# Kernel optimization log

Measured on AMD Instinct MI355X. Metric: run time of the kernel, lower is better.

The kernel has to match this reference:

```python
import jax, jax.numpy as jnp
import numpy as np

U1, U2, FEAT = 24, 48, 16
LN_EPS = 1e-3  # tf.keras LayerNormalization default


def _ln(x, gamma, beta):
    mu = jnp.mean(x, axis=-1, keepdims=True)
    var = jnp.mean(jnp.square(x - mu), axis=-1, keepdims=True)
    return (x - mu) * jax.lax.rsqrt(var + LN_EPS) * gamma + beta


def setup_inputs() -> dict:
    key = jax.random.key(0)
    ks = jax.random.split(key, 8)
    B, T = 8192, 256
    sequence = jax.random.normal(ks[0], (B, T, FEAT), dtype=jnp.float32)
    s = 0.1
    return {
        "sequence": sequence,
        "W1": jax.random.normal(ks[1], (FEAT, U1), dtype=jnp.float32) * s,
        "b1": jnp.zeros((U1,), jnp.float32),
        "Wr1": jax.random.normal(ks[2], (U1, U1), dtype=jnp.float32) * s,
        "br1": jnp.zeros((U1,), jnp.float32),
        "g1": jnp.ones((U1,), jnp.float32),
        "be1": jnp.zeros((U1,), jnp.float32),
        "W2": jax.random.normal(ks[3], (U1, U2), dtype=jnp.float32) * s,
        "b2": jnp.zeros((U2,), jnp.float32),
        "Wr2": jax.random.normal(ks[4], (U2, U2), dtype=jnp.float32) * s,
        "br2": jnp.zeros((U2,), jnp.float32),
        "g2": jnp.ones((U2,), jnp.float32),
        "be2": jnp.zeros((U2,), jnp.float32),
        "Wout": jax.random.normal(ks[5], (U2, 1), dtype=jnp.float32) * s,
        "bout": jnp.zeros((1,), jnp.float32),
    }


def reference(sequence, W1, b1, Wr1, br1, g1, be1, W2, b2, Wr2, br2, g2, be2, Wout, bout):
    B = sequence.shape[0]
    xs = jnp.swapaxes(sequence, 0, 1)  # [T, B, F]

    def step(carry, inp):
        s1, s2 = carry
        x = inp @ W1 + b1 + s1
        ns1 = jnp.tanh(x @ Wr1 + br1)
        h = _ln(ns1, g1, be1)
        y = h @ W2 + b2 + s2
        ns2 = jnp.tanh(y @ Wr2 + br2)
        return (ns1, ns2), None

    init = (jnp.zeros((B, U1), sequence.dtype), jnp.zeros((B, U2), sequence.dtype))
    (s1, s2), _ = jax.lax.scan(step, init, xs)
    last_out = _ln(s2, g2, be2)  # output of final timestep (return_sequences=False)
    return jax.nn.sigmoid(last_out @ Wout + bout)  # [B, 1]
```

## Files before the change

kernel.cpp:

```cpp
#include <hip/hip_runtime.h>

#define T_STEPS 256
#define FEAT 16
#define U1 24
#define U2 48
#define ROWB 144
#define SLOTS 8

typedef short bf16x8 __attribute__((ext_vector_type(8)));
typedef float f32x4 __attribute__((ext_vector_type(4)));

__device__ __forceinline__ unsigned short f2bf(float f) {
    unsigned u = __float_as_uint(f);
    u += 0x7fffu + ((u >> 16) & 1u);
    return (unsigned short)(u >> 16);
}

#if defined(__has_builtin)
#if __has_builtin(__builtin_amdgcn_cvt_pk_bf16_f32)
#define HAVE_PKBF16 1
#endif
#endif

__device__ __forceinline__ unsigned pk2(float a, float b) {
#ifdef HAVE_PKBF16
    typedef __bf16 bf2 __attribute__((ext_vector_type(2)));
    union { bf2 v; unsigned u; } cv;
    cv.v = __builtin_amdgcn_cvt_pk_bf16_f32(a, b);
    return cv.u;
#else
    return (unsigned)f2bf(a) | ((unsigned)f2bf(b) << 16);
#endif
}
__device__ __forceinline__ float bfr(float x) {
    return __uint_as_float(((unsigned)f2bf(x)) << 16);
}
__device__ __forceinline__ float fast_tanh(float z) {
    return 1.0f - 2.0f / (1.0f + __expf(2.0f * z));
}

union FragU { bf16x8 v; unsigned u[4]; };

#define MFMA(A, B, C) __builtin_amdgcn_mfma_f32_16x16x32_bf16((A), (B), (C), 0, 0, 0)

__device__ __forceinline__ void bar_sync() {
    asm volatile("" ::: "memory");
    __builtin_amdgcn_s_waitcnt(0xC07F);
    __builtin_amdgcn_s_barrier();
    asm volatile("" ::: "memory");
}

__global__ __launch_bounds__(128) void rnn_kernel(
    const float* __restrict__ seq,
    const float* __restrict__ W1, const float* __restrict__ b1,
    const float* __restrict__ Wr1, const float* __restrict__ br1,
    const float* __restrict__ g1, const float* __restrict__ be1,
    const float* __restrict__ W2, const float* __restrict__ b2,
    const float* __restrict__ Wr2, const float* __restrict__ br2,
    const float* __restrict__ g2, const float* __restrict__ be2,
    const float* __restrict__ Wout, const float* __restrict__ bout,
    float* __restrict__ out)
{
    __shared__ __align__(16) unsigned char tr0[16 * ROWB];
    __shared__ __align__(16) unsigned char tr1[16 * ROWB];
    __shared__ __align__(16) unsigned char ring[SLOTS * 16 * ROWB];

    const int tid = threadIdx.x;
    const int w = tid >> 6;
    const int lane = tid & 63;
    const int j15 = lane & 15;
    const int g = lane >> 4;
    const f32x4 z4 = {0.f, 0.f, 0.f, 0.f};

    if (w == 0) {
        bf16x8 A1[2], A2[2];
#pragma unroll
        for (int t = 0; t < 2; ++t) {
            const int m = 16 * t + j15;
            FragU f1, f2;
#pragma unroll
            for (int j = 0; j < 8; ++j) {
                const int k = 8 * g + j;
                float v1 = 0.f, v2 = 0.f;
                if (m < U1) {
                    if (k < FEAT) v1 = W1[k * U1 + m];
                    else if (k == FEAT) v1 = b1[m];
                    if (k < U1) v2 = Wr1[k * U1 + m];
                    else if (k == U1) v2 = br1[m];
                } else if (m == U1 && k == FEAT) {
                    v1 = 1.f;
                }
                f1.v[j] = (short)f2bf(v1);
                f2.v[j] = (short)f2bf(v2);
            }
            A1[t] = f1.v; A2[t] = f2.v;
        }
        const unsigned cdw0 = (g == 2) ? 0x00003F80u : 0u;
        unsigned char* const xrow = tr0 + j15 * ROWB;

        const float* sp = seq + (size_t)(blockIdx.x * 16 + j15) * (T_STEPS * FEAT) + 8 * g;
        const bool ld = (lane < 32);

        f32x4 s1[2] = {z4, z4};

        auto pstep = [&](int t, const float4 ca, const float4 cb) {
            FragU inf;
            const unsigned p0 = pk2(ca.x, ca.y), p1 = pk2(ca.z, ca.w);
            const unsigned p2 = pk2(cb.x, cb.y), p3 = pk2(cb.z, cb.w);
            const bool lo = (g < 2);
            inf.u[0] = lo ? p0 : cdw0;
            inf.u[1] = lo ? p1 : 0u;
            inf.u[2] = lo ? p2 : 0u;
            inf.u[3] = lo ? p3 : 0u;

            const f32x4 x0 = MFMA(A1[0], inf.v, s1[0]);
            const f32x4 x1 = MFMA(A1[1], inf.v, s1[1]);

            *(uint2*)(xrow + 8 * g)      = make_uint2(pk2(x0[0], x0[1]), pk2(x0[2], x0[3]));
            *(uint2*)(xrow + 32 + 8 * g) = make_uint2(pk2(x1[0], x1[1]), pk2(x1[2], x1[3]));
            const bf16x8 xf = *(const bf16x8*)(xrow + 16 * g);

            const f32x4 d0 = MFMA(A2[0], xf, z4);
            const f32x4 d1 = MFMA(A2[1], xf, z4);
            float n1a[4], n1b[4], qa[4], qb[4];
#pragma unroll
            for (int r = 0; r < 4; ++r) {
                n1a[r] = fast_tanh(d0[r]); n1b[r] = fast_tanh(d1[r]);
                qa[r] = n1a[r] * n1a[r];   qb[r] = n1b[r] * n1b[r];
                s1[0][r] = n1a[r];         s1[1][r] = n1b[r];
            }
            unsigned char* rp = ring + ((size_t)(t & (SLOTS - 1)) * 16 + j15) * ROWB;
            *(uint2*)(rp + 8 * g)      = make_uint2(pk2(n1a[0], n1a[1]), pk2(n1a[2], n1a[3]));
            *(uint2*)(rp + 32 + 8 * g) = make_uint2(pk2(n1b[0], n1b[1]), pk2(n1b[2], n1b[3]));
            *(uint2*)(rp + 64 + 8 * g) = make_uint2(pk2(qa[0], qa[1]), pk2(qa[2], qa[3]));
            *(uint2*)(rp + 96 + 8 * g) = make_uint2(pk2(qb[0], qb[1]), pk2(qb[2], qb[3]));
        };

        float4 ca[4], cb[4], na[4], nb[4];
        if (ld) {
#pragma unroll
            for (int i = 0; i < 4; ++i) {
                ca[i] = *(const float4*)(sp + i * 16);
                cb[i] = *(const float4*)(sp + i * 16 + 4);
            }
        }
#pragma unroll 1
        for (int j = 0; j < 64; ++j) {
            const int jn = (j + 1 < 64) ? j + 1 : j;
            if (ld) {
#pragma unroll
                for (int i = 0; i < 4; ++i) {
                    na[i] = *(const float4*)(sp + (4 * jn + i) * 16);
                    nb[i] = *(const float4*)(sp + (4 * jn + i) * 16 + 4);
                }
            }
#pragma unroll
            for (int i = 0; i < 4; ++i) pstep(4 * j + i, ca[i], cb[i]);
            bar_sync();
#pragma unroll
            for (int i = 0; i < 4; ++i) { ca[i] = na[i]; cb[i] = nb[i]; }
        }
        bar_sync();
    } else {
        for (int i = lane; i < 16 * ROWB / 4; i += 64) ((unsigned*)tr1)[i] = 0u;
        if (lane < 16) *(unsigned short*)(tr1 + lane * ROWB + 96) = 0x3F80;

        bf16x8 A3a[4], A3b3, A4[3][2];
#pragma unroll
        for (int t = 0; t < 3; ++t) {
            const int m = 16 * t + j15;
            FragU f3, f4a, f4b;
#pragma unroll
            for (int j = 0; j < 8; ++j) {
                const int k = 8 * g + j;
                const float v3 = (k < U1) ? g1[k] * W2[k * U2 + m] : 0.f;
                const int kb = 32 + k;
                const float va = Wr2[k * U2 + m];
                const float vb = (kb < U2) ? Wr2[kb * U2 + m] : (kb == U2 ? br2[m] : 0.f);
                f3.v[j] = (short)f2bf(v3);
                f4a.v[j] = (short)f2bf(va);
                f4b.v[j] = (short)f2bf(vb);
            }
            A3a[t] = f3.v; A4[t][0] = f4a.v; A4[t][1] = f4b.v;
        }
        {
            FragU fa, fb;
#pragma unroll
            for (int j = 0; j < 8; ++j) {
                const int k = 8 * g + j;
                fa.v[j] = ((j15 & 3) == 0 && k < U1) ? (short)0x3F80 : (short)0;
                fb.v[j] = ((j15 & 3) == 1 && k < U1) ? (short)0x3F80 : (short)0;
            }
            A3a[3] = fa.v; A3b3 = fb.v;
        }
        float cC[12], dC[12];
#pragma unroll
        for (int i = 0; i < 12; ++i) {
            const int m = 16 * (i >> 2) + 4 * g + (i & 3);
            float cc = 0.f, dd = b2[m];
            for (int k = 0; k < U1; ++k) {
                const float wq = bfr(g1[k] * W2[k * U2 + m]);
                cc += wq;
                dd += be1[k] * W2[k * U2 + m];
            }
            cC[i] = cc; dC[i] = dd;
        }
        unsigned char* const yrow = tr1 + j15 * ROWB;
        f32x4 s2[3] = {z4, z4, z4};

        auto cstep = [&](int t) {
            const unsigned char* rp = ring + ((size_t)(t & (SLOTS - 1)) * 16 + j15) * ROWB;
            const bf16x8 hf0 = *(const bf16x8*)(rp + 16 * g);
            const bf16x8 hf1 = *(const bf16x8*)(rp + 64 + 16 * g);

            f32x4 sAcc = MFMA(A3a[3], hf0, z4);
            sAcc = MFMA(A3b3, hf1, sAcc);
            const f32x4 P0 = MFMA(A3a[0], hf0, z4);
            const f32x4 P1 = MFMA(A3a[1], hf0, z4);
            const f32x4 P2 = MFMA(A3a[2], hf0, z4);

            const float mu = sAcc[0] * (1.f / U1);
            const float var = sAcc[1] * (1.f / U1) - mu * mu;
            const float rs = rsqrtf(var + 1e-3f);

            float y[12];
#pragma unroll
            for (int r = 0; r < 4; ++r) {
                y[r]     = fmaf(rs, fmaf(-mu, cC[r],     P0[r]), dC[r]     + s2[0][r]);
                y[4 + r] = fmaf(rs, fmaf(-mu, cC[4 + r], P1[r]), dC[4 + r] + s2[1][r]);
                y[8 + r] = fmaf(rs, fmaf(-mu, cC[8 + r], P2[r]), dC[8 + r] + s2[2][r]);
            }

            *(uint2*)(yrow + 8 * g)      = make_uint2(pk2(y[0], y[1]), pk2(y[2], y[3]));
            *(uint2*)(yrow + 32 + 8 * g) = make_uint2(pk2(y[4], y[5]), pk2(y[6], y[7]));
            *(uint2*)(yrow + 64 + 8 * g) = make_uint2(pk2(y[8], y[9]), pk2(y[10], y[11]));
            const bf16x8 yf0 = *(const bf16x8*)(yrow + 16 * g);
            const bf16x8 yf1 = *(const bf16x8*)(yrow + 64 + 16 * g);

#pragma unroll
            for (int t3 = 0; t3 < 3; ++t3) {
                f32x4 e = MFMA(A4[t3][0], yf0, z4);
                e = MFMA(A4[t3][1], yf1, e);
#pragma unroll
                for (int r = 0; r < 4; ++r) s2[t3][r] = fast_tanh(e[r]);
            }
        };

        bar_sync();
#pragma unroll 1
        for (int j = 0; j < 64; ++j) {
#pragma unroll
            for (int i = 0; i < 4; ++i) cstep(4 * j + i);
            bar_sync();
        }

        float g2r[12], be2r[12], wor[12];
#pragma unroll
        for (int r = 0; r < 12; ++r) {
            const int n = 16 * (r >> 2) + 4 * g + (r & 3);
            g2r[r] = g2[n]; be2r[r] = be2[n]; wor[r] = Wout[n];
        }
        float sm = 0.f, sq = 0.f;
#pragma unroll
        for (int tt = 0; tt < 3; ++tt)
#pragma unroll
            for (int r = 0; r < 4; ++r) { const float v = s2[tt][r]; sm += v; sq += v * v; }
        sm += __shfl_xor(sm, 16, 64); sq += __shfl_xor(sq, 16, 64);
        sm += __shfl_xor(sm, 32, 64); sq += __shfl_xor(sq, 32, 64);
        const float mu = sm * (1.f / U2);
        const float var = sq * (1.f / U2) - mu * mu;
        const float rs = rsqrtf(var + 1e-3f);
        float p = 0.f;
#pragma unroll
        for (int tt = 0; tt < 3; ++tt)
#pragma unroll
            for (int r = 0; r < 4; ++r)
                p += ((s2[tt][r] - mu) * rs * g2r[4 * tt + r] + be2r[4 * tt + r]) * wor[4 * tt + r];
        p += __shfl_xor(p, 16, 64);
        p += __shfl_xor(p, 32, 64);
        if (lane < 16) {
            const float z = p + bout[0];
            out[blockIdx.x * 16 + lane] = 1.0f / (1.0f + __expf(-z));
        }
    }
}

extern "C" void kernel_launch(void* const* d_in, const int* in_sizes, int n_in,
                              void* d_out, int out_size, void* d_ws, size_t ws_size,
                              hipStream_t stream) {
    const float* seq  = (const float*)d_in[0];
    const float* W1   = (const float*)d_in[1];
    const float* b1   = (const float*)d_in[2];
    const float* Wr1  = (const float*)d_in[3];
    const float* br1  = (const float*)d_in[4];
    const float* g1   = (const float*)d_in[5];
    const float* be1  = (const float*)d_in[6];
    const float* W2   = (const float*)d_in[7];
    const float* b2   = (const float*)d_in[8];
    const float* Wr2  = (const float*)d_in[9];
    const float* br2  = (const float*)d_in[10];
    const float* g2   = (const float*)d_in[11];
    const float* be2  = (const float*)d_in[12];
    const float* Wout = (const float*)d_in[13];
    const float* bout = (const float*)d_in[14];
    float* out = (float*)d_out;

    const int B = in_sizes[0] / (T_STEPS * FEAT);
    const int grid = B / 16;
    rnn_kernel<<<grid, 128, 0, stream>>>(seq, W1, b1, Wr1, br1, g1, be1,
                                         W2, b2, Wr2, br2, g2, be2, Wout, bout, out);
}
```

Measured before the change: 352.6 us.

## Replace LDS transposes with ds_bpermute and move LN stats to producer wave

The per-step MFMA output-to-operand transposes for x and y, previously a write to LDS followed by a read back, are replaced with ds_bpermute lane shuffles and selects. The producer wave now computes the LayerNorm mean and rstd itself with cross-lane shuffles and writes them into the ring slot. The consumer wave therefore no longer runs two MFMAs to sum h and h² or needs the squared-h rows. The aim is to shorten the serial per-timestep dependency chain and cut LDS traffic, at the cost of more bpermute instructions and extra shuffle work on the producer wave.

```diff
diff --git a/kernel.cpp b/kernel.cpp
--- a/kernel.cpp
+++ b/kernel.cpp
@@ -4,8 +4,10 @@
 #define FEAT 16
 #define U1 24
 #define U2 48
+#define SLOTS 8
 #define ROWB 144
-#define SLOTS 8
+#define SLOT_B (16 * ROWB + 128)
+#define SUMS_OFF (16 * ROWB)
 
 typedef short bf16x8 __attribute__((ext_vector_type(8)));
 typedef float f32x4 __attribute__((ext_vector_type(4)));
@@ -29,7 +31,10 @@
     cv.v = __builtin_amdgcn_cvt_pk_bf16_f32(a, b);
     return cv.u;
 #else
-    return (unsigned)f2bf(a) | ((unsigned)f2bf(b) << 16);
+    unsigned ua = __float_as_uint(a), ub = __float_as_uint(b);
+    ua += 0x7fffu + ((ua >> 16) & 1u);
+    ub += 0x7fffu + ((ub >> 16) & 1u);
+    return __builtin_amdgcn_perm(ub, ua, 0x07060302);
 #endif
 }
 __device__ __forceinline__ float bfr(float x) {
@@ -37,6 +42,9 @@
 }
 __device__ __forceinline__ float fast_tanh(float z) {
     return 1.0f - 2.0f / (1.0f + __expf(2.0f * z));
+}
+__device__ __forceinline__ unsigned bpermu(int addr, unsigned v) {
+    return (unsigned)__builtin_amdgcn_ds_bpermute(addr, (int)v);
 }
 
 union FragU { bf16x8 v; unsigned u[4]; };
@@ -61,16 +69,18 @@
     const float* __restrict__ Wout, const float* __restrict__ bout,
     float* __restrict__ out)
 {
-    __shared__ __align__(16) unsigned char tr0[16 * ROWB];
-    __shared__ __align__(16) unsigned char tr1[16 * ROWB];
-    __shared__ __align__(16) unsigned char ring[SLOTS * 16 * ROWB];
+    __shared__ __align__(16) unsigned char ring[SLOTS * SLOT_B];
 
     const int tid = threadIdx.x;
     const int w = tid >> 6;
     const int lane = tid & 63;
     const int j15 = lane & 15;
     const int g = lane >> 4;
+    const bool lo = (g < 2);
     const f32x4 z4 = {0.f, 0.f, 0.f, 0.f};
+
+    const int aA = (j15 + 16 * (2 * (g & 1))) << 2;
+    const int aB = aA + 64;
 
     if (w == 0) {
         bf16x8 A1[2], A2[2];
@@ -96,7 +106,6 @@
             A1[t] = f1.v; A2[t] = f2.v;
         }
         const unsigned cdw0 = (g == 2) ? 0x00003F80u : 0u;
-        unsigned char* const xrow = tr0 + j15 * ROWB;
 
         const float* sp = seq + (size_t)(blockIdx.x * 16 + j15) * (T_STEPS * FEAT) + 8 * g;
         const bool ld = (lane < 32);
@@ -107,7 +116,6 @@
             FragU inf;
             const unsigned p0 = pk2(ca.x, ca.y), p1 = pk2(ca.z, ca.w);
             const unsigned p2 = pk2(cb.x, cb.y), p3 = pk2(cb.z, cb.w);
-            const bool lo = (g < 2);
             inf.u[0] = lo ? p0 : cdw0;
             inf.u[1] = lo ? p1 : 0u;
             inf.u[2] = lo ? p2 : 0u;
@@ -116,24 +124,45 @@
             const f32x4 x0 = MFMA(A1[0], inf.v, s1[0]);
             const f32x4 x1 = MFMA(A1[1], inf.v, s1[1]);
 
-            *(uint2*)(xrow + 8 * g)      = make_uint2(pk2(x0[0], x0[1]), pk2(x0[2], x0[3]));
-            *(uint2*)(xrow + 32 + 8 * g) = make_uint2(pk2(x1[0], x1[1]), pk2(x1[2], x1[3]));
-            const bf16x8 xf = *(const bf16x8*)(xrow + 16 * g);
-
-            const f32x4 d0 = MFMA(A2[0], xf, z4);
-            const f32x4 d1 = MFMA(A2[1], xf, z4);
-            float n1a[4], n1b[4], qa[4], qb[4];
+            const unsigned px00 = pk2(x0[0], x0[1]), px01 = pk2(x0[2], x0[3]);
+            const unsigned px10 = pk2(x1[0], x1[1]), px11 = pk2(x1[2], x1[3]);
+            const unsigned r00 = bpermu(aA, px00), r01 = bpermu(aA, px01);
+            const unsigned r02 = bpermu(aB, px00), r03 = bpermu(aB, px01);
+            const unsigned r10 = bpermu(aA, px10), r11 = bpermu(aA, px11);
+            const unsigned r12 = bpermu(aB, px10), r13 = bpermu(aB, px11);
+            FragU xf;
+            xf.u[0] = lo ? r00 : r10;
+            xf.u[1] = lo ? r01 : r11;
+            xf.u[2] = lo ? r02 : r12;
+            xf.u[3] = lo ? r03 : r13;
+
+            const f32x4 d0 = MFMA(A2[0], xf.v, z4);
+            const f32x4 d1 = MFMA(A2[1], xf.v, z4);
+            float n1a[4], n1b[4];
 #pragma unroll
             for (int r = 0; r < 4; ++r) {
                 n1a[r] = fast_tanh(d0[r]); n1b[r] = fast_tanh(d1[r]);
-                qa[r] = n1a[r] * n1a[r];   qb[r] = n1b[r] * n1b[r];
                 s1[0][r] = n1a[r];         s1[1][r] = n1b[r];
             }
-            unsigned char* rp = ring + ((size_t)(t & (SLOTS - 1)) * 16 + j15) * ROWB;
+
+            unsigned char* rp = ring + (size_t)(t & (SLOTS - 1)) * SLOT_B + (size_t)j15 * ROWB;
             *(uint2*)(rp + 8 * g)      = make_uint2(pk2(n1a[0], n1a[1]), pk2(n1a[2], n1a[3]));
             *(uint2*)(rp + 32 + 8 * g) = make_uint2(pk2(n1b[0], n1b[1]), pk2(n1b[2], n1b[3]));
-            *(uint2*)(rp + 64 + 8 * g) = make_uint2(pk2(qa[0], qa[1]), pk2(qa[2], qa[3]));
-            *(uint2*)(rp + 96 + 8 * g) = make_uint2(pk2(qb[0], qb[1]), pk2(qb[2], qb[3]));
+
+            float sm = 0.f, sq = 0.f;
+#pragma unroll
+            for (int r = 0; r < 4; ++r) {
+                sm += n1a[r] + n1b[r];
+                sq = fmaf(n1a[r], n1a[r], sq);
+                sq = fmaf(n1b[r], n1b[r], sq);
+            }
+            sm += __shfl_xor(sm, 16, 64); sq += __shfl_xor(sq, 16, 64);
+            sm += __shfl_xor(sm, 32, 64); sq += __shfl_xor(sq, 32, 64);
+            const float mu = sm * (1.f / U1);
+            const float rs = rsqrtf(sq * (1.f / U1) - mu * mu + 1e-3f);
+            if (lane < 16)
+                *(float2*)(ring + (size_t)(t & (SLOTS - 1)) * SLOT_B + SUMS_OFF + 8 * j15) =
+                    make_float2(mu, rs);
         };
 
         float4 ca[4], cb[4], na[4], nb[4];
@@ -162,10 +191,7 @@
         }
         bar_sync();
     } else {
-        for (int i = lane; i < 16 * ROWB / 4; i += 64) ((unsigned*)tr1)[i] = 0u;
-        if (lane < 16) *(unsigned short*)(tr1 + lane * ROWB + 96) = 0x3F80;
-
-        bf16x8 A3a[4], A3b3, A4[3][2];
+        bf16x8 A3a[3], A4[3][2];
 #pragma unroll
         for (int t = 0; t < 3; ++t) {
             const int m = 16 * t + j15;
@@ -183,45 +209,28 @@
             }
             A3a[t] = f3.v; A4[t][0] = f4a.v; A4[t][1] = f4b.v;
         }
-        {
-            FragU fa, fb;
-#pragma unroll
-            for (int j = 0; j < 8; ++j) {
-                const int k = 8 * g + j;
-                fa.v[j] = ((j15 & 3) == 0 && k < U1) ? (short)0x3F80 : (short)0;
-                fb.v[j] = ((j15 & 3) == 1 && k < U1) ? (short)0x3F80 : (short)0;
-            }
-            A3a[3] = fa.v; A3b3 = fb.v;
-        }
         float cC[12], dC[12];
 #pragma unroll
         for (int i = 0; i < 12; ++i) {
             const int m = 16 * (i >> 2) + 4 * g + (i & 3);
             float cc = 0.f, dd = b2[m];
             for (int k = 0; k < U1; ++k) {
-                const float wq = bfr(g1[k] * W2[k * U2 + m]);
-                cc += wq;
+                cc += bfr(g1[k] * W2[k * U2 + m]);
                 dd += be1[k] * W2[k * U2 + m];
             }
             cC[i] = cc; dC[i] = dd;
         }
-        unsigned char* const yrow = tr1 + j15 * ROWB;
         f32x4 s2[3] = {z4, z4, z4};
 
         auto cstep = [&](int t) {
-            const unsigned char* rp = ring + ((size_t)(t & (SLOTS - 1)) * 16 + j15) * ROWB;
-            const bf16x8 hf0 = *(const bf16x8*)(rp + 16 * g);
-            const bf16x8 hf1 = *(const bf16x8*)(rp + 64 + 16 * g);
-
-            f32x4 sAcc = MFMA(A3a[3], hf0, z4);
-            sAcc = MFMA(A3b3, hf1, sAcc);
+            const unsigned char* sb = ring + (size_t)(t & (SLOTS - 1)) * SLOT_B;
+            const bf16x8 hf0 = *(const bf16x8*)(sb + (size_t)j15 * ROWB + 16 * g);
+            const float2 ms = *(const float2*)(sb + SUMS_OFF + 8 * j15);
+
             const f32x4 P0 = MFMA(A3a[0], hf0, z4);
             const f32x4 P1 = MFMA(A3a[1], hf0, z4);
             const f32x4 P2 = MFMA(A3a[2], hf0, z4);
-
-            const float mu = sAcc[0] * (1.f / U1);
-            const float var = sAcc[1] * (1.f / U1) - mu * mu;
-            const float rs = rsqrtf(var + 1e-3f);
+            const float mu = ms.x, rs = ms.y;
 
             float y[12];
 #pragma unroll
@@ -231,16 +240,29 @@
                 y[8 + r] = fmaf(rs, fmaf(-mu, cC[8 + r], P2[r]), dC[8 + r] + s2[2][r]);
             }
 
-            *(uint2*)(yrow + 8 * g)      = make_uint2(pk2(y[0], y[1]), pk2(y[2], y[3]));
-            *(uint2*)(yrow + 32 + 8 * g) = make_uint2(pk2(y[4], y[5]), pk2(y[6], y[7]));
-            *(uint2*)(yrow + 64 + 8 * g) = make_uint2(pk2(y[8], y[9]), pk2(y[10], y[11]));
-            const bf16x8 yf0 = *(const bf16x8*)(yrow + 16 * g);
-            const bf16x8 yf1 = *(const bf16x8*)(yrow + 64 + 16 * g);
+            const unsigned py00 = pk2(y[0], y[1]),  py01 = pk2(y[2], y[3]);
+            const unsigned py10 = pk2(y[4], y[5]),  py11 = pk2(y[6], y[7]);
+            const unsigned py20 = pk2(y[8], y[9]),  py21 = pk2(y[10], y[11]);
+            const unsigned r00 = bpermu(aA, py00), r01 = bpermu(aA, py01);
+            const unsigned r02 = bpermu(aB, py00), r03 = bpermu(aB, py01);
+            const unsigned r10 = bpermu(aA, py10), r11 = bpermu(aA, py11);
+            const unsigned r12 = bpermu(aB, py10), r13 = bpermu(aB, py11);
+            const unsigned q0  = bpermu(aA, py20), q1  = bpermu(aA, py21);
+            const unsigned q2  = bpermu(aB, py20), q3  = bpermu(aB, py21);
+            FragU yf0, yf1;
+            yf0.u[0] = lo ? r00 : r10;
+            yf0.u[1] = lo ? r01 : r11;
+            yf0.u[2] = lo ? r02 : r12;
+            yf0.u[3] = lo ? r03 : r13;
+            yf1.u[0] = lo ? q0 : (g == 2 ? 0x00003F80u : 0u);
+            yf1.u[1] = lo ? q1 : 0u;
+            yf1.u[2] = lo ? q2 : 0u;
+            yf1.u[3] = lo ? q3 : 0u;
 
 #pragma unroll
             for (int t3 = 0; t3 < 3; ++t3) {
-                f32x4 e = MFMA(A4[t3][0], yf0, z4);
-                e = MFMA(A4[t3][1], yf1, e);
+                f32x4 e = MFMA(A4[t3][0], yf0.v, z4);
+                e = MFMA(A4[t3][1], yf1.v, e);
 #pragma unroll
                 for (int r = 0; r < 4; ++r) s2[t3][r] = fast_tanh(e[r]);
             }
```

New measurement: 481.2 us. +36.5%, slower.

## Move layer-1 LN stats to producer wave and use fast tanh intrinsics

Applied to the files above, without the earlier changes.

The producer wave now computes the LayerNorm mean and rstd of the layer-1 state with cross-lane shuffles and writes them to a small shared-memory area. The consumer wave reads these values instead of running two extra MFMAs on a squared-state copy, and the producer no longer writes that squared copy. The ring is restructured as an 8-slot double-buffer with fixed slot indices and register double-buffered input loads. tanh, sigmoid and rsqrt switch to raw exp2/rcp/rsq intrinsics. This shifts shuffle work onto the producer's critical path and slightly lowers precision.

```diff
diff --git a/kernel.cpp b/kernel.cpp
--- a/kernel.cpp
+++ b/kernel.cpp
@@ -5,7 +5,9 @@
 #define U1 24
 #define U2 48
 #define ROWB 144
-#define SLOTS 8
+#define SLOT_ROWS (16 * ROWB)
+#define SUMS_BASE (8 * SLOT_ROWS)
+#define RING_BYTES (SUMS_BASE + 8 * 128)
 
 typedef short bf16x8 __attribute__((ext_vector_type(8)));
 typedef float f32x4 __attribute__((ext_vector_type(4)));
@@ -29,14 +31,40 @@
     cv.v = __builtin_amdgcn_cvt_pk_bf16_f32(a, b);
     return cv.u;
 #else
-    return (unsigned)f2bf(a) | ((unsigned)f2bf(b) << 16);
+    unsigned ua = __float_as_uint(a), ub = __float_as_uint(b);
+    ua += 0x7fffu + ((ua >> 16) & 1u);
+    ub += 0x7fffu + ((ub >> 16) & 1u);
+    return __builtin_amdgcn_perm(ub, ua, 0x07060302);
 #endif
 }
 __device__ __forceinline__ float bfr(float x) {
     return __uint_as_float(((unsigned)f2bf(x)) << 16);
 }
+
+__device__ __forceinline__ float rcp_fast(float x) {
+#if __has_builtin(__builtin_amdgcn_rcpf)
+    return __builtin_amdgcn_rcpf(x);
+#else
+    return 1.0f / x;
+#endif
+}
+__device__ __forceinline__ float exp2_fast(float x) {
+#if __has_builtin(__builtin_amdgcn_exp2f)
+    return __builtin_amdgcn_exp2f(x);
+#else
+    return exp2f(x);
+#endif
+}
+__device__ __forceinline__ float rsq_fast(float x) {
+#if __has_builtin(__builtin_amdgcn_rsqf)
+    return __builtin_amdgcn_rsqf(x);
+#else
+    return rsqrtf(x);
+#endif
+}
 __device__ __forceinline__ float fast_tanh(float z) {
-    return 1.0f - 2.0f / (1.0f + __expf(2.0f * z));
+    const float e = exp2_fast(2.885390081777927f * z);
+    return fmaf(-2.0f, rcp_fast(1.0f + e), 1.0f);
 }
 
 union FragU { bf16x8 v; unsigned u[4]; };
@@ -61,9 +89,9 @@
     const float* __restrict__ Wout, const float* __restrict__ bout,
     float* __restrict__ out)
 {
+    __shared__ __align__(16) unsigned char ring[RING_BYTES];
     __shared__ __align__(16) unsigned char tr0[16 * ROWB];
     __shared__ __align__(16) unsigned char tr1[16 * ROWB];
-    __shared__ __align__(16) unsigned char ring[SLOTS * 16 * ROWB];
 
     const int tid = threadIdx.x;
     const int w = tid >> 6;
@@ -96,76 +124,94 @@
             A1[t] = f1.v; A2[t] = f2.v;
         }
         const unsigned cdw0 = (g == 2) ? 0x00003F80u : 0u;
-        unsigned char* const xrow = tr0 + j15 * ROWB;
+        const bool lo = (g < 2);
+        unsigned char* const xw = tr0 + (size_t)j15 * ROWB + 8 * g;
+        const unsigned char* const xr = tr0 + (size_t)j15 * ROWB + 16 * g;
+        unsigned char* const nw = ring + (size_t)j15 * ROWB + 8 * g;
+        float2* const sw = (float2*)(ring + SUMS_BASE + 8 * j15);
 
         const float* sp = seq + (size_t)(blockIdx.x * 16 + j15) * (T_STEPS * FEAT) + 8 * g;
         const bool ld = (lane < 32);
 
+        float4 cA[4], cB[4], nA[4], nB[4];
+        if (!ld) {
+#pragma unroll
+            for (int i = 0; i < 4; ++i) {
+                cA[i] = make_float4(0.f, 0.f, 0.f, 0.f); cB[i] = cA[i];
+                nA[i] = cA[i]; nB[i] = cA[i];
+            }
+        }
+        auto load4 = [&](float4* A, float4* Bv, int gidx) {
+            if (ld) {
+                const float* q = sp + (size_t)gidx * 64;
+#pragma unroll
+                for (int i = 0; i < 4; ++i) {
+                    A[i] = *(const float4*)(q + 16 * i);
+                    Bv[i] = *(const float4*)(q + 16 * i + 4);
+                }
+            }
+        };
+
         f32x4 s1[2] = {z4, z4};
 
-        auto pstep = [&](int t, const float4 ca, const float4 cb) {
+        auto pstep = [&](const int s, const float4 ca, const float4 cb) {
             FragU inf;
-            const unsigned p0 = pk2(ca.x, ca.y), p1 = pk2(ca.z, ca.w);
-            const unsigned p2 = pk2(cb.x, cb.y), p3 = pk2(cb.z, cb.w);
-            const bool lo = (g < 2);
-            inf.u[0] = lo ? p0 : cdw0;
-            inf.u[1] = lo ? p1 : 0u;
-            inf.u[2] = lo ? p2 : 0u;
-            inf.u[3] = lo ? p3 : 0u;
+            inf.u[0] = lo ? pk2(ca.x, ca.y) : cdw0;
+            inf.u[1] = pk2(ca.z, ca.w);
+            inf.u[2] = pk2(cb.x, cb.y);
+            inf.u[3] = pk2(cb.z, cb.w);
 
             const f32x4 x0 = MFMA(A1[0], inf.v, s1[0]);
             const f32x4 x1 = MFMA(A1[1], inf.v, s1[1]);
 
-            *(uint2*)(xrow + 8 * g)      = make_uint2(pk2(x0[0], x0[1]), pk2(x0[2], x0[3]));
-            *(uint2*)(xrow + 32 + 8 * g) = make_uint2(pk2(x1[0], x1[1]), pk2(x1[2], x1[3]));
-            const bf16x8 xf = *(const bf16x8*)(xrow + 16 * g);
+            *(uint2*)(xw)      = make_uint2(pk2(x0[0], x0[1]), pk2(x0[2], x0[3]));
+            *(uint2*)(xw + 32) = make_uint2(pk2(x1[0], x1[1]), pk2(x1[2], x1[3]));
+            const bf16x8 xf = *(const bf16x8*)(xr);
 
             const f32x4 d0 = MFMA(A2[0], xf, z4);
             const f32x4 d1 = MFMA(A2[1], xf, z4);
-            float n1a[4], n1b[4], qa[4], qb[4];
+            float n1a[4], n1b[4];
 #pragma unroll
             for (int r = 0; r < 4; ++r) {
                 n1a[r] = fast_tanh(d0[r]); n1b[r] = fast_tanh(d1[r]);
-                qa[r] = n1a[r] * n1a[r];   qb[r] = n1b[r] * n1b[r];
                 s1[0][r] = n1a[r];         s1[1][r] = n1b[r];
             }
-            unsigned char* rp = ring + ((size_t)(t & (SLOTS - 1)) * 16 + j15) * ROWB;
-            *(uint2*)(rp + 8 * g)      = make_uint2(pk2(n1a[0], n1a[1]), pk2(n1a[2], n1a[3]));
-            *(uint2*)(rp + 32 + 8 * g) = make_uint2(pk2(n1b[0], n1b[1]), pk2(n1b[2], n1b[3]));
-            *(uint2*)(rp + 64 + 8 * g) = make_uint2(pk2(qa[0], qa[1]), pk2(qa[2], qa[3]));
-            *(uint2*)(rp + 96 + 8 * g) = make_uint2(pk2(qb[0], qb[1]), pk2(qb[2], qb[3]));
+            *(uint2*)(nw + s * SLOT_ROWS)      = make_uint2(pk2(n1a[0], n1a[1]), pk2(n1a[2], n1a[3]));
+            *(uint2*)(nw + s * SLOT_ROWS + 32) = make_uint2(pk2(n1b[0], n1b[1]), pk2(n1b[2], n1b[3]));
+
+            float sm = 0.f, sq = 0.f;
+#pragma unroll
+            for (int r = 0; r < 4; ++r) {
+                sm += n1a[r] + n1b[r];
+                sq = fmaf(n1a[r], n1a[r], sq);
+                sq = fmaf(n1b[r], n1b[r], sq);
+            }
+            sm += __shfl_xor(sm, 16, 64); sq += __shfl_xor(sq, 16, 64);
+            sm += __shfl_xor(sm, 32, 64); sq += __shfl_xor(sq, 32, 64);
+            const float mu = sm * (1.f / U1);
+            const float rs = rsq_fast(sq * (1.f / U1) - mu * mu + 1e-3f);
+            if (lane < 16) sw[s * 16] = make_float2(mu, rs);
         };
 
-        float4 ca[4], cb[4], na[4], nb[4];
-        if (ld) {
-#pragma unroll
-            for (int i = 0; i < 4; ++i) {
-                ca[i] = *(const float4*)(sp + i * 16);
-                cb[i] = *(const float4*)(sp + i * 16 + 4);
-            }
-        }
+        load4(cA, cB, 0);
+        load4(nA, nB, 1);
 #pragma unroll 1
-        for (int j = 0; j < 64; ++j) {
-            const int jn = (j + 1 < 64) ? j + 1 : j;
-            if (ld) {
-#pragma unroll
-                for (int i = 0; i < 4; ++i) {
-                    na[i] = *(const float4*)(sp + (4 * jn + i) * 16);
-                    nb[i] = *(const float4*)(sp + (4 * jn + i) * 16 + 4);
-                }
-            }
-#pragma unroll
-            for (int i = 0; i < 4; ++i) pstep(4 * j + i, ca[i], cb[i]);
+        for (int j = 0; j < 32; ++j) {
+            pstep(0, cA[0], cB[0]); pstep(1, cA[1], cB[1]);
+            pstep(2, cA[2], cB[2]); pstep(3, cA[3], cB[3]);
+            load4(cA, cB, (2 * j + 2 < 64) ? 2 * j + 2 : 63);
             bar_sync();
-#pragma unroll
-            for (int i = 0; i < 4; ++i) { ca[i] = na[i]; cb[i] = nb[i]; }
+            pstep(4, nA[0], nB[0]); pstep(5, nA[1], nB[1]);
+            pstep(6, nA[2], nB[2]); pstep(7, nA[3], nB[3]);
+            load4(nA, nB, (2 * j + 3 < 64) ? 2 * j + 3 : 63);
+            bar_sync();
         }
         bar_sync();
     } else {
         for (int i = lane; i < 16 * ROWB / 4; i += 64) ((unsigned*)tr1)[i] = 0u;
         if (lane < 16) *(unsigned short*)(tr1 + lane * ROWB + 96) = 0x3F80;
 
-        bf16x8 A3a[4], A3b3, A4[3][2];
+        bf16x8 A3a[3], A4[3][2];
 #pragma unroll
         for (int t = 0; t < 3; ++t) {
             const int m = 16 * t + j15;
@@ -183,45 +229,32 @@
             }
             A3a[t] = f3.v; A4[t][0] = f4a.v; A4[t][1] = f4b.v;
         }
-        {
-            FragU fa, fb;
-#pragma unroll
-            for (int j = 0; j < 8; ++j) {
-                const int k = 8 * g + j;
-                fa.v[j] = ((j15 & 3) == 0 && k < U1) ? (short)0x3F80 : (short)0;
-                fb.v[j] = ((j15 & 3) == 1 && k < U1) ? (short)0x3F80 : (short)0;
-            }
-            A3a[3] = fa.v; A3b3 = fb.v;
-        }
         float cC[12], dC[12];
 #pragma unroll
         for (int i = 0; i < 12; ++i) {
             const int m = 16 * (i >> 2) + 4 * g + (i & 3);
             float cc = 0.f, dd = b2[m];
             for (int k = 0; k < U1; ++k) {
-                const float wq = bfr(g1[k] * W2[k * U2 + m]);
-                cc += wq;
+                cc += bfr(g1[k] * W2[k * U2 + m]);
                 dd += be1[k] * W2[k * U2 + m];
             }
             cC[i] = cc; dC[i] = dd;
         }
-        unsigned char* const yrow = tr1 + j15 * ROWB;
+        const unsigned char* const nf = ring + (size_t)j15 * ROWB + 16 * g;
+        const float2* const msb = (const float2*)(ring + SUMS_BASE + 8 * j15);
+        unsigned char* const yw = tr1 + (size_t)j15 * ROWB + 8 * g;
+        const unsigned char* const yr = tr1 + (size_t)j15 * ROWB + 16 * g;
+
         f32x4 s2[3] = {z4, z4, z4};
 
-        auto cstep = [&](int t) {
-            const unsigned char* rp = ring + ((size_t)(t & (SLOTS - 1)) * 16 + j15) * ROWB;
-            const bf16x8 hf0 = *(const bf16x8*)(rp + 16 * g);
-            const bf16x8 hf1 = *(const bf16x8*)(rp + 64 + 16 * g);
-
-            f32x4 sAcc = MFMA(A3a[3], hf0, z4);
-            sAcc = MFMA(A3b3, hf1, sAcc);
+        auto cstep = [&](const int s) {
+            const bf16x8 hf0 = *(const bf16x8*)(nf + s * SLOT_ROWS);
+            const float2 ms = msb[s * 16];
+
             const f32x4 P0 = MFMA(A3a[0], hf0, z4);
             const f32x4 P1 = MFMA(A3a[1], hf0, z4);
             const f32x4 P2 = MFMA(A3a[2], hf0, z4);
-
-            const float mu = sAcc[0] * (1.f / U1);
-            const float var = sAcc[1] * (1.f / U1) - mu * mu;
-            const float rs = rsqrtf(var + 1e-3f);
+            const float mu = ms.x, rs = ms.y;
 
             float y[12];
 #pragma unroll
@@ -231,11 +264,11 @@
                 y[8 + r] = fmaf(rs, fmaf(-mu, cC[8 + r], P2[r]), dC[8 + r] + s2[2][r]);
             }
 
-            *(uint2*)(yrow + 8 * g)      = make_uint2(pk2(y[0], y[1]), pk2(y[2], y[3]));
-            *(uint2*)(yrow + 32 + 8 * g) = make_uint2(pk2(y[4], y[5]), pk2(y[6], y[7]));
-            *(uint2*)(yrow + 64 + 8 * g) = make_uint2(pk2(y[8], y[9]), pk2(y[10], y[11]));
-            const bf16x8 yf0 = *(const bf16x8*)(yrow + 16 * g);
-            const bf16x8 yf1 = *(const bf16x8*)(yrow + 64 + 16 * g);
+            *(uint2*)(yw)      = make_uint2(pk2(y[0], y[1]), pk2(y[2], y[3]));
+            *(uint2*)(yw + 32) = make_uint2(pk2(y[4], y[5]), pk2(y[6], y[7]));
+            *(uint2*)(yw + 64) = make_uint2(pk2(y[8], y[9]), pk2(y[10], y[11]));
+            const bf16x8 yf0 = *(const bf16x8*)(yr);
+            const bf16x8 yf1 = *(const bf16x8*)(yr + 64);
 
 #pragma unroll
             for (int t3 = 0; t3 < 3; ++t3) {
@@ -248,9 +281,10 @@
 
         bar_sync();
 #pragma unroll 1
-        for (int j = 0; j < 64; ++j) {
-#pragma unroll
-            for (int i = 0; i < 4; ++i) cstep(4 * j + i);
+        for (int j = 0; j < 32; ++j) {
+            cstep(0); cstep(1); cstep(2); cstep(3);
+            bar_sync();
+            cstep(4); cstep(5); cstep(6); cstep(7);
             bar_sync();
         }
 
@@ -269,7 +303,7 @@
         sm += __shfl_xor(sm, 32, 64); sq += __shfl_xor(sq, 32, 64);
         const float mu = sm * (1.f / U2);
         const float var = sq * (1.f / U2) - mu * mu;
-        const float rs = rsqrtf(var + 1e-3f);
+        const float rs = rsq_fast(var + 1e-3f);
         float p = 0.f;
 #pragma unroll
         for (int tt = 0; tt < 3; ++tt)
@@ -280,7 +314,7 @@
         p += __shfl_xor(p, 32, 64);
         if (lane < 16) {
             const float z = p + bout[0];
-            out[blockIdx.x * 16 + lane] = 1.0f / (1.0f + __expf(-z));
+            out[blockIdx.x * 16 + lane] = rcp_fast(1.0f + exp2_fast(-1.4426950408889634f * z));
         }
     }
 }
```

After: 390.1 us. 1.11x slower.
